# Kernel optimization log

Hardware: AMD Instinct MI355X
Metric: run time of the kernel (lower is better)

## Reference

```python
import jax, jax.numpy as jnp
import numpy as np

H = 32                         # LSTM_size
K = 3                          # k_value
NK, ND, NU = 4 * K + 2, K, K   # kernel / down / up step counts
T = NK + ND + NU
NEG = -1e9                     # finite mask value (avoids -inf NaNs)


def setup_inputs() -> dict:
    key = jax.random.key(0)
    ks = jax.random.split(key, 12)
    u = lambda k, s: jax.random.uniform(k, s, jnp.float32, -0.1, 0.1)
    return {
        "w_ih": u(ks[0], (4 * H, H)),
        "w_hh": u(ks[1], (4 * H, H)),
        "b_ih": u(ks[2], (4 * H,)),
        "b_hh": u(ks[3], (4 * H,)),
        "g_emb": u(ks[4], (1, H)),
        "emb_kernel": u(ks[5], (8, H)),
        "emb_down": u(ks[6], (3, H)),
        "emb_up": u(ks[7], (3, H)),
        "w_kernel": u(ks[8], (8, H)),
        "w_down": u(ks[9], (3, H)),
        "w_up": u(ks[10], (3, H)),
        "uniform_noise": jax.random.uniform(ks[11], (T, 8), jnp.float32),
    }


def _pad8(w):
    # zero-pad a [n<=8, H] table/head to [8, H]
    return jnp.pad(w, ((0, 8 - w.shape[0]), (0, 0)))


def _forward(w_ih, w_hh, b_ih, b_hh, g_emb, emb_kernel, emb_down, emb_up,
             w_kernel, w_down, w_up, uniform_noise):
    # Per-step projection heads [T, 8, H]; 3-class heads zero-padded to 8 and masked.
    proj = jnp.concatenate([
        jnp.broadcast_to(w_kernel, (NK, 8, H)),
        jnp.broadcast_to(_pad8(w_down), (ND, 8, H)),
        jnp.broadcast_to(_pad8(w_up), (NU, 8, H)),
    ])
    # Per-step embedding table used to embed the sampled action for the NEXT step.
    emb = jnp.concatenate([
        jnp.broadcast_to(emb_kernel, (NK, 8, H)),
        jnp.broadcast_to(_pad8(emb_down), (ND, 8, H)),
        jnp.broadcast_to(_pad8(emb_up), (NU, 8, H)),
    ])
    m3 = jnp.array([1, 1, 1, 0, 0, 0, 0, 0], dtype=bool)
    mask = jnp.concatenate([
        jnp.ones((NK, 8), dtype=bool),
        jnp.broadcast_to(m3, (ND, 8)),
        jnp.broadcast_to(m3, (NU, 8)),
    ])
    # Gumbel-max categorical sampling noise.
    gumbel = -jnp.log(-jnp.log(uniform_noise * (1.0 - 1e-6) + 1e-7))

    def step(carry, xs):
        h, c, x = carry                                   # h, c, x: [H]
        Wp, Et, msk, g = xs
        # Torch LSTM cell: gates = W_ih x + b_ih + W_hh h + b_hh, order i,f,g,o
        gates = w_ih @ x + b_ih + w_hh @ h + b_hh         # [4H]
        i, f, gg, o = jnp.split(gates, 4)
        c = jax.nn.sigmoid(f) * c + jax.nn.sigmoid(i) * jnp.tanh(gg)
        h = jax.nn.sigmoid(o) * jnp.tanh(c)
        logits = jnp.where(msk, Wp @ h, NEG)              # [8]
        logp = jax.nn.log_softmax(logits)
        s = jnp.argmax(logits + g)                        # Categorical sample
        p = jnp.where(msk, jnp.exp(logp), 0.0)
        ent = -jnp.sum(p * jnp.where(msk, logp, 0.0))
        return (h, c, Et[s]), (logp[s], ent, s)

    init = (jnp.zeros((H,), jnp.float32), jnp.zeros((H,), jnp.float32), g_emb[0])
    _, (lps, ents, samples) = jax.lax.scan(step, init, (proj, emb, mask, gumbel))
    # stats = [sample_log_prob, sample_entropy]
    return jnp.stack([jnp.sum(lps), jnp.sum(ents)]), samples


def reference(w_ih, w_hh, b_ih, b_hh, g_emb, emb_kernel, emb_down, emb_up,
              w_kernel, w_down, w_up, uniform_noise):
    return _forward(w_ih, w_hh, b_ih, b_hh, g_emb, emb_kernel, emb_down, emb_up,
                    w_kernel, w_down, w_up, uniform_noise)
```

## Files before the change

kernel.cpp:

```cpp
#include <hip/hip_runtime.h>

#define HH 32
#define TT 20

typedef float v2f __attribute__((ext_vector_type(2)));

#define LOG2E  1.4426950408889634f
#define LN2    0.6931471805599453f

__device__ __forceinline__ float fsig(float x) {
    return __builtin_amdgcn_rcpf(1.0f + __builtin_amdgcn_exp2f(-x * LOG2E));
}
__device__ __forceinline__ float ftanh(float x) {
    return 1.0f - 2.0f * __builtin_amdgcn_rcpf(1.0f + __builtin_amdgcn_exp2f(x * (2.0f * LOG2E)));
}

__global__ __launch_bounds__(64, 1) void controller_kernel(
    const float* __restrict__ w_ih,
    const float* __restrict__ w_hh,
    const float* __restrict__ b_ih,
    const float* __restrict__ b_hh,
    const float* __restrict__ g_emb,
    const float* __restrict__ emb_kernel,
    const float* __restrict__ emb_down,
    const float* __restrict__ emb_up,
    const float* __restrict__ w_kernel,
    const float* __restrict__ w_down,
    const float* __restrict__ w_up,
    const float* __restrict__ noise,
    float* __restrict__ out)
{
    const int t   = threadIdx.x;
    const int q   = t & 31;
    const int cls = t & 7;

    __shared__ __align__(16) float emb_s[15 * 32];
    __shared__ __align__(16) float Gv[15 * 64 * 4];
    __shared__ __align__(16) float h_s[32];
    __shared__ __align__(16) float gum_s[TT * 8];

    for (int i = t; i < 15 * 32; i += 64) {
        const int r = i >> 5, j = i & 31;
        float v;
        if (r < 8)       v = emb_kernel[r * 32 + j];
        else if (r < 11) v = emb_down[(r - 8) * 32 + j];
        else if (r < 14) v = emb_up[(r - 11) * 32 + j];
        else             v = g_emb[j];
        emb_s[i] = v;
    }
    for (int i = t; i < TT * 8; i += 64) {
        const float u = noise[i];
        gum_s[i] = -logf(-logf(u * (1.0f - 1e-6f) + 1e-7f));
    }

    float bias[4];
#pragma unroll
    for (int g = 0; g < 4; ++g) bias[g] = b_ih[q + 32 * g] + b_hh[q + 32 * g];

    {
        v2f wtmp[64];
#pragma unroll
        for (int g = 0; g < 4; ++g) {
            const float4* p = (const float4*)(w_ih + (q + 32 * g) * HH);
#pragma unroll
            for (int k8 = 0; k8 < 8; ++k8) {
                const float4 a = p[k8];
                wtmp[g * 16 + 2 * k8]     = (v2f){a.x, a.y};
                wtmp[g * 16 + 2 * k8 + 1] = (v2f){a.z, a.w};
            }
        }
        __syncthreads();
        for (int e = 0; e < 15; ++e) {
            const float4* ep = (const float4*)(emb_s + e * 32);
            v2f er[16];
#pragma unroll
            for (int k8 = 0; k8 < 8; ++k8) {
                const float4 a = ep[k8];
                er[2 * k8]     = (v2f){a.x, a.y};
                er[2 * k8 + 1] = (v2f){a.z, a.w};
            }
            v2f g0 = {0.f,0.f}, g1 = {0.f,0.f}, g2 = {0.f,0.f}, g3 = {0.f,0.f};
#pragma unroll
            for (int k = 0; k < 16; ++k) {
                g0 += wtmp[k]      * er[k];
                g1 += wtmp[16 + k] * er[k];
                g2 += wtmp[32 + k] * er[k];
                g3 += wtmp[48 + k] * er[k];
            }
            *(float4*)(Gv + (e * 64 + t) * 4) =
                make_float4(bias[0] + g0.x + g0.y, bias[1] + g1.x + g1.y,
                            bias[2] + g2.x + g2.y, bias[3] + g3.x + g3.y);
        }
    }
    __builtin_amdgcn_sched_barrier(0);

    v2f whh[64];
#pragma unroll
    for (int g = 0; g < 4; ++g) {
        const float4* p = (const float4*)(w_hh + (q + 32 * g) * HH);
#pragma unroll
        for (int k8 = 0; k8 < 8; ++k8) {
            const float4 a = p[k8];
            whh[g * 16 + 2 * k8]     = (v2f){a.x, a.y};
            whh[g * 16 + 2 * k8 + 1] = (v2f){a.z, a.w};
        }
    }
    v2f hk[16], hd[16], hu[16];
#pragma unroll
    for (int k8 = 0; k8 < 8; ++k8) {
        const float4 a = ((const float4*)(w_kernel + cls * 32))[k8];
        hk[2 * k8] = (v2f){a.x, a.y}; hk[2 * k8 + 1] = (v2f){a.z, a.w};
        float4 b = make_float4(0.f, 0.f, 0.f, 0.f);
        float4 c = make_float4(0.f, 0.f, 0.f, 0.f);
        if (cls < 3) {
            b = ((const float4*)(w_down + cls * 32))[k8];
            c = ((const float4*)(w_up + cls * 32))[k8];
        }
        hd[2 * k8] = (v2f){b.x, b.y}; hd[2 * k8 + 1] = (v2f){b.z, b.w};
        hu[2 * k8] = (v2f){c.x, c.y}; hu[2 * k8 + 1] = (v2f){c.z, c.w};
    }

    v2f hreg[16];
#pragma unroll
    for (int k = 0; k < 16; ++k) hreg[k] = (v2f){0.f, 0.f};
    float c_reg = 0.0f;
    float4 G4 = *(const float4*)(Gv + (14 * 64 + t) * 4);
    float lp_sum = 0.0f, ent_sum = 0.0f;

    for (int step = 0; step < TT; ++step) {
        const float4 gu0 = *(const float4*)(gum_s + step * 8);
        const float4 gu1 = *(const float4*)(gum_s + step * 8 + 4);

        v2f ai0 = {0.f,0.f}, ai1 = {0.f,0.f}, af0 = {0.f,0.f}, af1 = {0.f,0.f};
        v2f ag0 = {0.f,0.f}, ag1 = {0.f,0.f}, ao0 = {0.f,0.f}, ao1 = {0.f,0.f};
#pragma unroll
        for (int k = 0; k < 16; k += 2) {
            ai0 += whh[k]      * hreg[k];  ai1 += whh[k + 1]      * hreg[k + 1];
            af0 += whh[16 + k] * hreg[k];  af1 += whh[16 + k + 1] * hreg[k + 1];
            ag0 += whh[32 + k] * hreg[k];  ag1 += whh[32 + k + 1] * hreg[k + 1];
            ao0 += whh[48 + k] * hreg[k];  ao1 += whh[48 + k + 1] * hreg[k + 1];
        }
        const float ai = G4.x + ((ai0.x + ai0.y) + (ai1.x + ai1.y));
        const float af = G4.y + ((af0.x + af0.y) + (af1.x + af1.y));
        const float ag = G4.z + ((ag0.x + ag0.y) + (ag1.x + ag1.y));
        const float ao = G4.w + ((ao0.x + ao0.y) + (ao1.x + ao1.y));

        const float ig = fsig(ai), fg = fsig(af), gg = ftanh(ag), og = fsig(ao);
        c_reg = fg * c_reg + ig * gg;
        const float hn = og * ftanh(c_reg);
        if (t < 32) h_s[t] = hn;
        __syncthreads();

#pragma unroll
        for (int k8 = 0; k8 < 8; ++k8) {
            const float4 hv = ((const float4*)h_s)[k8];
            hreg[2 * k8]     = (v2f){hv.x, hv.y};
            hreg[2 * k8 + 1] = (v2f){hv.z, hv.w};
        }

        const int n = (step < 14) ? 8 : 3;
        v2f s0 = {0.f,0.f}, s1 = {0.f,0.f};
        if (step < 14) {
#pragma unroll
            for (int k = 0; k < 16; k += 2) { s0 += hk[k] * hreg[k]; s1 += hk[k+1] * hreg[k+1]; }
        } else if (step < 17) {
#pragma unroll
            for (int k = 0; k < 16; k += 2) { s0 += hd[k] * hreg[k]; s1 += hd[k+1] * hreg[k+1]; }
        } else {
#pragma unroll
            for (int k = 0; k < 16; k += 2) { s0 += hu[k] * hreg[k]; s1 += hu[k+1] * hreg[k+1]; }
        }
        float l = (s0.x + s0.y) + (s1.x + s1.y);
        l = (cls < n) ? l : -1e9f;

        float lv[8];
#pragma unroll
        for (int k = 0; k < 8; ++k) lv[k] = __shfl(l, k);

        float S = 0.0f, Tm = 0.0f;
#pragma unroll
        for (int k = 0; k < 8; ++k) {
            const float e = __builtin_amdgcn_exp2f(lv[k] * LOG2E);
            S  += e;
            Tm += e * lv[k];
        }
        const float gum[8] = {gu0.x, gu0.y, gu0.z, gu0.w, gu1.x, gu1.y, gu1.z, gu1.w};
        int   idx = 0;
        float bv  = lv[0] + gum[0];
        float bl  = lv[0];
#pragma unroll
        for (int k = 1; k < 8; ++k) {
            const float v = lv[k] + gum[k];
            const bool take = v > bv;
            bv  = take ? v : bv;
            idx = take ? k : idx;
            bl  = take ? lv[k] : bl;
        }
        const float lse = __builtin_amdgcn_logf(S) * LN2;
        lp_sum  += bl - lse;
        ent_sum += lse - Tm * __builtin_amdgcn_rcpf(S);
        if (t == 0) out[2 + step] = (float)idx;

        const int nrb = ((step + 1) < 14) ? 0 : (((step + 1) < 17) ? 8 : 11);
        int nrow = nrb + idx;
        if (nrow > 14) nrow = 14;
        G4 = *(const float4*)(Gv + (nrow * 64 + t) * 4);
    }

    if (t == 0) {
        out[0] = lp_sum;
        out[1] = ent_sum;
    }
}

extern "C" void kernel_launch(void* const* d_in, const int* in_sizes, int n_in,
                              void* d_out, int out_size, void* d_ws, size_t ws_size,
                              hipStream_t stream) {
    (void)in_sizes; (void)n_in; (void)out_size; (void)d_ws; (void)ws_size;
    const float* w_ih       = (const float*)d_in[0];
    const float* w_hh       = (const float*)d_in[1];
    const float* b_ih       = (const float*)d_in[2];
    const float* b_hh       = (const float*)d_in[3];
    const float* g_emb      = (const float*)d_in[4];
    const float* emb_kernel = (const float*)d_in[5];
    const float* emb_down   = (const float*)d_in[6];
    const float* emb_up     = (const float*)d_in[7];
    const float* w_kernel   = (const float*)d_in[8];
    const float* w_down     = (const float*)d_in[9];
    const float* w_up       = (const float*)d_in[10];
    const float* noise      = (const float*)d_in[11];
    float* out = (float*)d_out;

    hipLaunchKernelGGL(controller_kernel, dim3(1), dim3(64), 0, stream,
                       w_ih, w_hh, b_ih, b_hh, g_emb, emb_kernel, emb_down,
                       emb_up, w_kernel, w_down, w_up, noise, out);
}
```

Baseline: 98.68 us.

## Keep precomputed input-gate table in registers and select via predicated tree

```diff
diff --git a/kernel.cpp b/kernel.cpp
--- a/kernel.cpp
+++ b/kernel.cpp
@@ -35,16 +35,15 @@
     const int cls = t & 7;
 
     __shared__ __align__(16) float emb_s[15 * 32];
-    __shared__ __align__(16) float Gv[15 * 64 * 4];
     __shared__ __align__(16) float h_s[32];
     __shared__ __align__(16) float gum_s[TT * 8];
 
     for (int i = t; i < 15 * 32; i += 64) {
         const int r = i >> 5, j = i & 31;
         float v;
-        if (r < 8)       v = emb_kernel[r * 32 + j];
-        else if (r < 11) v = emb_down[(r - 8) * 32 + j];
-        else if (r < 14) v = emb_up[(r - 11) * 32 + j];
+        if (r < 8)       v = emb_kernel[i];
+        else if (r < 11) v = emb_down[i - 8 * 32];
+        else if (r < 14) v = emb_up[i - 11 * 32];
         else             v = g_emb[j];
         emb_s[i] = v;
     }
@@ -57,39 +56,35 @@
 #pragma unroll
     for (int g = 0; g < 4; ++g) bias[g] = b_ih[q + 32 * g] + b_hh[q + 32 * g];
 
+    float4 Gall[15];
     {
-        v2f wtmp[64];
+        v2f wih[64];
 #pragma unroll
         for (int g = 0; g < 4; ++g) {
             const float4* p = (const float4*)(w_ih + (q + 32 * g) * HH);
 #pragma unroll
             for (int k8 = 0; k8 < 8; ++k8) {
                 const float4 a = p[k8];
-                wtmp[g * 16 + 2 * k8]     = (v2f){a.x, a.y};
-                wtmp[g * 16 + 2 * k8 + 1] = (v2f){a.z, a.w};
+                wih[g * 16 + 2 * k8]     = (v2f){a.x, a.y};
+                wih[g * 16 + 2 * k8 + 1] = (v2f){a.z, a.w};
             }
         }
         __syncthreads();
+#pragma unroll
         for (int e = 0; e < 15; ++e) {
             const float4* ep = (const float4*)(emb_s + e * 32);
-            v2f er[16];
+            v2f g0 = {0.f,0.f}, g1 = {0.f,0.f}, g2 = {0.f,0.f}, g3 = {0.f,0.f};
 #pragma unroll
             for (int k8 = 0; k8 < 8; ++k8) {
                 const float4 a = ep[k8];
-                er[2 * k8]     = (v2f){a.x, a.y};
-                er[2 * k8 + 1] = (v2f){a.z, a.w};
+                const v2f e0 = {a.x, a.y}, e1 = {a.z, a.w};
+                g0 += wih[2*k8]      * e0;  g0 += wih[2*k8+1]      * e1;
+                g1 += wih[16+2*k8]   * e0;  g1 += wih[16+2*k8+1]   * e1;
+                g2 += wih[32+2*k8]   * e0;  g2 += wih[32+2*k8+1]   * e1;
+                g3 += wih[48+2*k8]   * e0;  g3 += wih[48+2*k8+1]   * e1;
             }
-            v2f g0 = {0.f,0.f}, g1 = {0.f,0.f}, g2 = {0.f,0.f}, g3 = {0.f,0.f};
-#pragma unroll
-            for (int k = 0; k < 16; ++k) {
-                g0 += wtmp[k]      * er[k];
-                g1 += wtmp[16 + k] * er[k];
-                g2 += wtmp[32 + k] * er[k];
-                g3 += wtmp[48 + k] * er[k];
-            }
-            *(float4*)(Gv + (e * 64 + t) * 4) =
-                make_float4(bias[0] + g0.x + g0.y, bias[1] + g1.x + g1.y,
-                            bias[2] + g2.x + g2.y, bias[3] + g3.x + g3.y);
+            Gall[e] = make_float4(bias[0] + g0.x + g0.y, bias[1] + g1.x + g1.y,
+                                  bias[2] + g2.x + g2.y, bias[3] + g3.x + g3.y);
         }
     }
     __builtin_amdgcn_sched_barrier(0);
@@ -109,66 +104,61 @@
 #pragma unroll
     for (int k8 = 0; k8 < 8; ++k8) {
         const float4 a = ((const float4*)(w_kernel + cls * 32))[k8];
-        hk[2 * k8] = (v2f){a.x, a.y}; hk[2 * k8 + 1] = (v2f){a.z, a.w};
-        float4 b = make_float4(0.f, 0.f, 0.f, 0.f);
-        float4 c = make_float4(0.f, 0.f, 0.f, 0.f);
+        hk[2*k8] = (v2f){a.x, a.y}; hk[2*k8+1] = (v2f){a.z, a.w};
+        float4 b = make_float4(0.f,0.f,0.f,0.f), c = make_float4(0.f,0.f,0.f,0.f);
         if (cls < 3) {
             b = ((const float4*)(w_down + cls * 32))[k8];
             c = ((const float4*)(w_up + cls * 32))[k8];
         }
-        hd[2 * k8] = (v2f){b.x, b.y}; hd[2 * k8 + 1] = (v2f){b.z, b.w};
-        hu[2 * k8] = (v2f){c.x, c.y}; hu[2 * k8 + 1] = (v2f){c.z, c.w};
+        hd[2*k8] = (v2f){b.x, b.y}; hd[2*k8+1] = (v2f){b.z, b.w};
+        hu[2*k8] = (v2f){c.x, c.y}; hu[2*k8+1] = (v2f){c.z, c.w};
     }
 
     v2f hreg[16];
 #pragma unroll
     for (int k = 0; k < 16; ++k) hreg[k] = (v2f){0.f, 0.f};
-    float c_reg = 0.0f;
-    float4 G4 = *(const float4*)(Gv + (14 * 64 + t) * 4);
-    float lp_sum = 0.0f, ent_sum = 0.0f;
-
+    float  c_reg = 0.0f;
+    float4 G4 = Gall[14];
+    float  lp_sum = 0.0f, ent_sum = 0.0f;
+
+#pragma unroll
     for (int step = 0; step < TT; ++step) {
-        const float4 gu0 = *(const float4*)(gum_s + step * 8);
-        const float4 gu1 = *(const float4*)(gum_s + step * 8 + 4);
-
-        v2f ai0 = {0.f,0.f}, ai1 = {0.f,0.f}, af0 = {0.f,0.f}, af1 = {0.f,0.f};
-        v2f ag0 = {0.f,0.f}, ag1 = {0.f,0.f}, ao0 = {0.f,0.f}, ao1 = {0.f,0.f};
+        v2f ai0={0.f,0.f}, af0={0.f,0.f}, ag0={0.f,0.f}, ao0={0.f,0.f};
+        v2f ai1={0.f,0.f}, af1={0.f,0.f}, ag1={0.f,0.f}, ao1={0.f,0.f};
 #pragma unroll
         for (int k = 0; k < 16; k += 2) {
-            ai0 += whh[k]      * hreg[k];  ai1 += whh[k + 1]      * hreg[k + 1];
-            af0 += whh[16 + k] * hreg[k];  af1 += whh[16 + k + 1] * hreg[k + 1];
-            ag0 += whh[32 + k] * hreg[k];  ag1 += whh[32 + k + 1] * hreg[k + 1];
-            ao0 += whh[48 + k] * hreg[k];  ao1 += whh[48 + k + 1] * hreg[k + 1];
-        }
-        const float ai = G4.x + ((ai0.x + ai0.y) + (ai1.x + ai1.y));
-        const float af = G4.y + ((af0.x + af0.y) + (af1.x + af1.y));
-        const float ag = G4.z + ((ag0.x + ag0.y) + (ag1.x + ag1.y));
-        const float ao = G4.w + ((ao0.x + ao0.y) + (ao1.x + ao1.y));
+            ai0 += whh[k]      * hreg[k];  ai1 += whh[k+1]      * hreg[k+1];
+            af0 += whh[16+k]   * hreg[k];  af1 += whh[16+k+1]   * hreg[k+1];
+            ag0 += whh[32+k]   * hreg[k];  ag1 += whh[32+k+1]   * hreg[k+1];
+            ao0 += whh[48+k]   * hreg[k];  ao1 += whh[48+k+1]   * hreg[k+1];
+        }
+        const float ai = G4.x + ((ai0.x+ai0.y) + (ai1.x+ai1.y));
+        const float af = G4.y + ((af0.x+af0.y) + (af1.x+af1.y));
+        const float ag = G4.z + ((ag0.x+ag0.y) + (ag1.x+ag1.y));
+        const float ao = G4.w + ((ao0.x+ao0.y) + (ao1.x+ao1.y));
 
         const float ig = fsig(ai), fg = fsig(af), gg = ftanh(ag), og = fsig(ao);
         c_reg = fg * c_reg + ig * gg;
         const float hn = og * ftanh(c_reg);
-        if (t < 32) h_s[t] = hn;
+        h_s[q] = hn;
         __syncthreads();
-
 #pragma unroll
         for (int k8 = 0; k8 < 8; ++k8) {
             const float4 hv = ((const float4*)h_s)[k8];
-            hreg[2 * k8]     = (v2f){hv.x, hv.y};
-            hreg[2 * k8 + 1] = (v2f){hv.z, hv.w};
+            hreg[2*k8] = (v2f){hv.x, hv.y}; hreg[2*k8+1] = (v2f){hv.z, hv.w};
         }
 
         const int n = (step < 14) ? 8 : 3;
         v2f s0 = {0.f,0.f}, s1 = {0.f,0.f};
         if (step < 14) {
 #pragma unroll
-            for (int k = 0; k < 16; k += 2) { s0 += hk[k] * hreg[k]; s1 += hk[k+1] * hreg[k+1]; }
+            for (int k = 0; k < 16; k += 2) { s0 += hk[k]*hreg[k]; s1 += hk[k+1]*hreg[k+1]; }
         } else if (step < 17) {
 #pragma unroll
-            for (int k = 0; k < 16; k += 2) { s0 += hd[k] * hreg[k]; s1 += hd[k+1] * hreg[k+1]; }
+            for (int k = 0; k < 16; k += 2) { s0 += hd[k]*hreg[k]; s1 += hd[k+1]*hreg[k+1]; }
         } else {
 #pragma unroll
-            for (int k = 0; k < 16; k += 2) { s0 += hu[k] * hreg[k]; s1 += hu[k+1] * hreg[k+1]; }
+            for (int k = 0; k < 16; k += 2) { s0 += hu[k]*hreg[k]; s1 += hu[k+1]*hreg[k+1]; }
         }
         float l = (s0.x + s0.y) + (s1.x + s1.y);
         l = (cls < n) ? l : -1e9f;
@@ -181,30 +171,44 @@
 #pragma unroll
         for (int k = 0; k < 8; ++k) {
             const float e = __builtin_amdgcn_exp2f(lv[k] * LOG2E);
-            S  += e;
-            Tm += e * lv[k];
-        }
-        const float gum[8] = {gu0.x, gu0.y, gu0.z, gu0.w, gu1.x, gu1.y, gu1.z, gu1.w};
-        int   idx = 0;
-        float bv  = lv[0] + gum[0];
-        float bl  = lv[0];
-#pragma unroll
-        for (int k = 1; k < 8; ++k) {
-            const float v = lv[k] + gum[k];
-            const bool take = v > bv;
-            bv  = take ? v : bv;
-            idx = take ? k : idx;
-            bl  = take ? lv[k] : bl;
-        }
+            S += e; Tm += e * lv[k];
+        }
+        const float4 gA = ((const float4*)(gum_s + step * 8))[0];
+        const float4 gB = ((const float4*)(gum_s + step * 8))[1];
+        const float v0 = lv[0]+gA.x, v1 = lv[1]+gA.y, v2 = lv[2]+gA.z, v3 = lv[3]+gA.w;
+        const float v4 = lv[4]+gB.x, v5 = lv[5]+gB.y, v6 = lv[6]+gB.z, v7 = lv[7]+gB.w;
+        const bool ta = v1 > v0;  const float va = ta?v1:v0;  int ia = ta?1:0;  const float la = ta?lv[1]:lv[0];
+        const bool tb = v3 > v2;  const float vb = tb?v3:v2;  int ib = tb?3:2;  const float lb = tb?lv[3]:lv[2];
+        const bool tc = v5 > v4;  const float vc = tc?v5:v4;  int ic = tc?5:4;  const float lc = tc?lv[5]:lv[4];
+        const bool td = v7 > v6;  const float vd = td?v7:v6;  int id_= td?7:6;  const float ld = td?lv[7]:lv[6];
+        const bool tab = vb > va; const float vab = tab?vb:va; const int iab = tab?ib:ia; const float lab = tab?lb:la;
+        const bool tcd = vd > vc; const float vcd = tcd?vd:vc; const int icd = tcd?id_:ic; const float lcd = tcd?ld:lc;
+        const bool tf  = vcd > vab;
+        const int   idx = tf ? icd : iab;
+        const float bl  = tf ? lcd : lab;
+
         const float lse = __builtin_amdgcn_logf(S) * LN2;
         lp_sum  += bl - lse;
         ent_sum += lse - Tm * __builtin_amdgcn_rcpf(S);
         if (t == 0) out[2 + step] = (float)idx;
 
-        const int nrb = ((step + 1) < 14) ? 0 : (((step + 1) < 17) ? 8 : 11);
-        int nrow = nrb + idx;
-        if (nrow > 14) nrow = 14;
-        G4 = *(const float4*)(Gv + (nrow * 64 + t) * 4);
+        if (step < TT - 1) {
+            if (step < 14) {
+                const float4 s01 = (idx & 1) ? Gall[1] : Gall[0];
+                const float4 s23 = (idx & 1) ? Gall[3] : Gall[2];
+                const float4 s45 = (idx & 1) ? Gall[5] : Gall[4];
+                const float4 s67 = (idx & 1) ? Gall[7] : Gall[6];
+                const float4 sA  = (idx & 2) ? s23 : s01;
+                const float4 sB  = (idx & 2) ? s67 : s45;
+                G4 = (idx & 4) ? sB : sA;
+            } else if (step < 17) {
+                const float4 a = (idx == 1) ? Gall[9] : Gall[8];
+                G4 = (idx == 2) ? Gall[10] : a;
+            } else {
+                const float4 a = (idx == 1) ? Gall[12] : Gall[11];
+                G4 = (idx == 2) ? Gall[13] : a;
+            }
+        }
     }
 
     if (t == 0) {
```

Result: slower. 151.9 us (+54.0%).
